# Kernel tuning notes

Measured on AMD Instinct MI355X. Metric: run time of the kernel, lower is better.

## Reference

```python
import jax, jax.numpy as jnp
import numpy as np

EPS = 1e-6      # torch F.pairwise_distance default eps (added to the difference)
MARGIN = 0.5


def setup_inputs() -> dict:
    key = jax.random.key(0)
    k1, k2 = jax.random.split(key)
    batch = jax.random.normal(k1, (8192, 1024), dtype=jnp.float32)
    positive = jax.random.normal(k2, (1024,), dtype=jnp.float32)
    return {"batch": batch, "positive": positive}


def _loss(batch, positive):
    n, d = batch.shape
    # torch pairwise_distance(x, y) = ||x - y + eps||_2, so
    # ||a - b + eps||^2 = ||a||^2 + ||b||^2 - 2 a.b + 2*eps*(sum(a) - sum(b)) + d*eps^2
    sq = jnp.sum(batch * batch, axis=-1)                 # [n]
    dots = batch @ batch.T                               # [n, n] GEMM
    sums = jnp.sum(batch, axis=-1)                       # [n]
    d2 = (sq[:, None] + sq[None, :] - 2.0 * dots
          + 2.0 * EPS * (sums[:, None] - sums[None, :]) + d * EPS * EPS)
    # exclude self (the python loop concatenates batch[:i], batch[i+1:])
    neg_inf = jnp.asarray(-jnp.inf, d2.dtype)
    d2_masked = jnp.where(jnp.eye(n, dtype=bool), neg_inf, d2)
    max_neg = jnp.sqrt(jnp.maximum(jnp.max(d2_masked, axis=-1), 0.0))  # [n]
    # distance anchor -> positive (with torch eps convention)
    diff = batch - positive[None, :] + EPS
    pos_dist = jnp.sqrt(jnp.sum(diff * diff, axis=-1))   # [n]
    losses = jax.nn.relu(pos_dist - max_neg + MARGIN)    # [n]
    # anchors exactly equal to the positive are skipped in the original loop
    valid = ~jnp.all(batch == positive[None, :], axis=-1)
    cnt = jnp.sum(valid.astype(losses.dtype))
    return jnp.sum(jnp.where(valid, losses, 0.0)) / cnt


def reference(batch, positive):
    return _loss(batch, positive)
```

## Files before the change

kernel.cpp:

```cpp
#include <hip/hip_runtime.h>
#include <hip/hip_bf16.h>


#define NROWS 8192
#define DIM   1024
#define BT    256
#define BK    64
#define NKT   (DIM / BK)
#define NBT   (NROWS / BT)
#define NTRI  (NBT * (NBT + 1) / 2)

constexpr float EPS = 1e-6f;
constexpr float MARGIN = 0.5f;

typedef __attribute__((ext_vector_type(8))) short short8;
typedef __attribute__((ext_vector_type(4))) float f32x4;

__device__ __forceinline__ unsigned short f2bf_rne(float f) {
    unsigned u = __float_as_uint(f);
    u += 0x7fffu + ((u >> 16) & 1u);
    return (unsigned short)(u >> 16);
}

__global__ void prep_kernel(const float* __restrict__ X, const float* __restrict__ P,
                            unsigned short* __restrict__ Xb,
                            float* __restrict__ cj, float* __restrict__ basei,
                            float* __restrict__ posd, int* __restrict__ valid)
{
    const int tid  = threadIdx.x;
    const int w    = tid >> 6;
    const int lane = tid & 63;
    const int row  = blockIdx.x * 4 + w;
    const float* xr = X + (size_t)row * DIM;

    float sq = 0.f, sm = 0.f, pd = 0.f;
    bool eq = true;
    #pragma unroll
    for (int it = 0; it < 4; ++it) {
        const int idx = it * 256 + lane * 4;
        const float4 x = *(const float4*)(xr + idx);
        const float4 p = *(const float4*)(P + idx);
        sq += x.x*x.x + x.y*x.y + x.z*x.z + x.w*x.w;
        sm += x.x + x.y + x.z + x.w;
        const float d0 = x.x - p.x + EPS, d1 = x.y - p.y + EPS;
        const float d2 = x.z - p.z + EPS, d3 = x.w - p.w + EPS;
        pd += d0*d0 + d1*d1 + d2*d2 + d3*d3;
        eq = eq && (x.x == p.x) && (x.y == p.y) && (x.z == p.z) && (x.w == p.w);
        ushort4 b;
        b.x = f2bf_rne(x.x); b.y = f2bf_rne(x.y); b.z = f2bf_rne(x.z); b.w = f2bf_rne(x.w);
        *(ushort4*)(Xb + (size_t)row * DIM + idx) = b;
    }
    #pragma unroll
    for (int off = 32; off >= 1; off >>= 1) {
        sq += __shfl_xor(sq, off);
        sm += __shfl_xor(sm, off);
        pd += __shfl_xor(pd, off);
    }
    const bool alleq = __all(eq);
    if (lane == 0) {
        cj[row]    = sq - 2.f * EPS * sm;
        basei[row] = sq + 2.f * EPS * sm + (float)DIM * EPS * EPS;
        posd[row]  = sqrtf(pd);
        valid[row] = alleq ? 0 : 1;
    }
}

__global__ __launch_bounds__(512, 2) void gemm_max_kernel(
        const unsigned short* __restrict__ Xb,
        const float* __restrict__ cj,
        float* __restrict__ partmax)
{
    __shared__ alignas(16) unsigned short lds[2][4][8192];
    __shared__ float partrow[4][BT];
    __shared__ float partcol[2][BT];

    const int tid  = threadIdx.x;
    const int lane = tid & 63;
    const int wid  = tid >> 6;
    const int wm   = wid >> 2;
    const int wn   = wid & 3;
    const int l15  = lane & 15;
    const int lk   = lane >> 4;
    const int cx0  = lk ^ (l15 & 7);
    const int cx1  = (4 + lk) ^ (l15 & 7);

    const int t0 = (blockIdx.x & 7) * (NTRI / 8) + (blockIdx.x >> 3);
    int bm = (int)(32.5f - sqrtf(1056.25f - 2.f * (float)t0));
    if (bm < 0) bm = 0;
    if (bm > NBT - 1) bm = NBT - 1;
    while (bm > 0 && (65 * bm - bm * bm) / 2 > t0) --bm;
    while ((65 * (bm + 1) - (bm + 1) * (bm + 1)) / 2 <= t0) ++bm;
    const int bn = bm + (t0 - (65 * bm - bm * bm) / 2);
    const bool diag = (bm == bn);
    const int Mbase = bm * BT, Nbase = bn * BT;

    f32x4 acc[8][4];
    #pragma unroll
    for (int m = 0; m < 8; ++m)
        #pragma unroll
        for (int n = 0; n < 4; ++n)
            acc[m][n] = (f32x4){0.f, 0.f, 0.f, 0.f};

    #define STAGE(BUF, SLOT, GBASE, KT) do {                                                  \
        _Pragma("unroll")                                                                     \
        for (int inst_ = 0; inst_ < 2; ++inst_) {                                             \
            const int q_ = inst_ * 512 + tid;                                                 \
            const int r_ = q_ >> 3;                                                           \
            const int c_ = (q_ & 7) ^ (r_ & 7);                                               \
            const unsigned short* src_ = Xb + (size_t)((GBASE) + r_) * DIM + (KT) * BK + c_ * 8; \
            unsigned short* dst_ = &lds[BUF][SLOT][(inst_ * 512 + wid * 64) * 8];             \
            __builtin_amdgcn_global_load_lds((const __attribute__((address_space(1))) void*)src_, \
                                             (__attribute__((address_space(3))) void*)dst_, 16, 0, 0); \
        }                                                                                     \
    } while (0)

    STAGE(0, 0, Mbase, 0); STAGE(0, 1, Mbase + 128, 0);
    STAGE(0, 2, Nbase, 0); STAGE(0, 3, Nbase + 128, 0);
    STAGE(1, 0, Mbase, 1); STAGE(1, 1, Mbase + 128, 1);
    STAGE(1, 2, Nbase, 1); STAGE(1, 3, Nbase + 128, 1);
    asm volatile("s_waitcnt vmcnt(8)" ::: "memory");
    __builtin_amdgcn_s_barrier();
    __builtin_amdgcn_sched_barrier(0);

    const int cl0 = (wn & 1) * 64;

    short8 bf0[4], bf1[4], af[8];
    {
        const unsigned short* B0 = &lds[0][2 + (wn >> 1)][0];
        #pragma unroll
        for (int nt = 0; nt < 2; ++nt) {
            bf0[nt * 2]     = *(const short8*)(B0 + ((cl0 + nt * 16 + l15) * 8 + cx0) * 8);
            bf0[nt * 2 + 1] = *(const short8*)(B0 + ((cl0 + nt * 16 + l15) * 8 + cx1) * 8);
        }
    }

    for (int kt = 0; kt < NKT; ++kt) {
        const int b = kt & 1;
        const unsigned short* Ah = &lds[b][wm][0];
        const unsigned short* Bh = &lds[b][2 + (wn >> 1)][0];
        const unsigned short* Bn = &lds[b ^ 1][2 + (wn >> 1)][0];
        const bool st = (kt + 2 < NKT);
        const int kp = kt + 2;

        #pragma unroll
        for (int mt = 0; mt < 4; ++mt) {
            af[mt * 2]     = *(const short8*)(Ah + ((mt * 16 + l15) * 8 + cx0) * 8);
            af[mt * 2 + 1] = *(const short8*)(Ah + ((mt * 16 + l15) * 8 + cx1) * 8);
        }
        __builtin_amdgcn_s_setprio(1);
        #pragma unroll
        for (int ks = 0; ks < 2; ++ks)
            #pragma unroll
            for (int mt = 0; mt < 4; ++mt)
                #pragma unroll
                for (int nt = 0; nt < 2; ++nt)
                    acc[mt][nt] = __builtin_amdgcn_mfma_f32_16x16x32_bf16(af[mt*2+ks], bf0[nt*2+ks], acc[mt][nt], 0, 0, 0);
        __builtin_amdgcn_s_setprio(0);
        __builtin_amdgcn_s_barrier();

        #pragma unroll
        for (int nt = 0; nt < 2; ++nt) {
            bf1[nt * 2]     = *(const short8*)(Bh + ((cl0 + 32 + nt * 16 + l15) * 8 + cx0) * 8);
            bf1[nt * 2 + 1] = *(const short8*)(Bh + ((cl0 + 32 + nt * 16 + l15) * 8 + cx1) * 8);
        }
        __builtin_amdgcn_s_setprio(1);
        #pragma unroll
        for (int ks = 0; ks < 2; ++ks)
            #pragma unroll
            for (int mt = 0; mt < 4; ++mt)
                #pragma unroll
                for (int nt = 0; nt < 2; ++nt)
                    acc[mt][2+nt] = __builtin_amdgcn_mfma_f32_16x16x32_bf16(af[mt*2+ks], bf1[nt*2+ks], acc[mt][2+nt], 0, 0, 0);
        __builtin_amdgcn_s_setprio(0);
        __builtin_amdgcn_s_barrier();

        #pragma unroll
        for (int mt = 0; mt < 4; ++mt) {
            af[mt * 2]     = *(const short8*)(Ah + ((64 + mt * 16 + l15) * 8 + cx0) * 8);
            af[mt * 2 + 1] = *(const short8*)(Ah + ((64 + mt * 16 + l15) * 8 + cx1) * 8);
        }
        if (st) { STAGE(b, 2, Nbase, kp); STAGE(b, 3, Nbase + 128, kp); }
        __builtin_amdgcn_s_setprio(1);
        #pragma unroll
        for (int ks = 0; ks < 2; ++ks)
            #pragma unroll
            for (int mt = 0; mt < 4; ++mt)
                #pragma unroll
                for (int nt = 0; nt < 2; ++nt)
                    acc[4+mt][2+nt] = __builtin_amdgcn_mfma_f32_16x16x32_bf16(af[mt*2+ks], bf1[nt*2+ks], acc[4+mt][2+nt], 0, 0, 0);
        __builtin_amdgcn_s_setprio(0);
        __builtin_amdgcn_s_barrier();

        if (st) { STAGE(b, 0, Mbase, kp); STAGE(b, 1, Mbase + 128, kp); }
        __builtin_amdgcn_s_setprio(1);
        #pragma unroll
        for (int ks = 0; ks < 2; ++ks)
            #pragma unroll
            for (int mt = 0; mt < 4; ++mt)
                #pragma unroll
                for (int nt = 0; nt < 2; ++nt)
                    acc[4+mt][nt] = __builtin_amdgcn_mfma_f32_16x16x32_bf16(af[mt*2+ks], bf0[nt*2+ks], acc[4+mt][nt], 0, 0, 0);
        __builtin_amdgcn_s_setprio(0);

        if (kt <= NKT - 3)      asm volatile("s_waitcnt vmcnt(8)" ::: "memory");
        else                    asm volatile("s_waitcnt vmcnt(0)" ::: "memory");
        if (kt < NKT - 1) {
            #pragma unroll
            for (int nt = 0; nt < 2; ++nt) {
                bf0[nt * 2]     = *(const short8*)(Bn + ((cl0 + nt * 16 + l15) * 8 + cx0) * 8);
                bf0[nt * 2 + 1] = *(const short8*)(Bn + ((cl0 + nt * 16 + l15) * 8 + cx1) * 8);
            }
        }
        __builtin_amdgcn_s_barrier();
        __builtin_amdgcn_sched_barrier(0);
    }
    #undef STAGE

    float cv[4];
    #pragma unroll
    for (int n = 0; n < 4; ++n)
        cv[n] = cj[Nbase + wn * 64 + n * 16 + l15];

    #pragma unroll
    for (int m = 0; m < 8; ++m) {
        #pragma unroll
        for (int r = 0; r < 4; ++r) {
            const int lrow = wm * 128 + m * 16 + lk * 4 + r;
            float v = -__builtin_inff();
            #pragma unroll
            for (int n = 0; n < 4; ++n) {
                float val = cv[n] - 2.f * acc[m][n][r];
                if (diag && lrow == wn * 64 + n * 16 + l15) val = -__builtin_inff();
                v = fmaxf(v, val);
            }
            #pragma unroll
            for (int off = 8; off >= 1; off >>= 1)
                v = fmaxf(v, __shfl_xor(v, off));
            if (l15 == 0) partrow[wn][lrow] = v;
        }
    }

    if (!diag) {
        float vt[4];
        #pragma unroll
        for (int n = 0; n < 4; ++n) vt[n] = -__builtin_inff();
        #pragma unroll
        for (int m = 0; m < 8; ++m) {
            #pragma unroll
            for (int r = 0; r < 4; ++r) {
                const float ci = cj[Mbase + wm * 128 + m * 16 + lk * 4 + r];
                #pragma unroll
                for (int n = 0; n < 4; ++n)
                    vt[n] = fmaxf(vt[n], ci - 2.f * acc[m][n][r]);
            }
        }
        #pragma unroll
        for (int n = 0; n < 4; ++n) {
            vt[n] = fmaxf(vt[n], __shfl_xor(vt[n], 16));
            vt[n] = fmaxf(vt[n], __shfl_xor(vt[n], 32));
            if (lk == 0) partcol[wm][wn * 64 + n * 16 + l15] = vt[n];
        }
    }
    __syncthreads();

    if (tid < BT) {
        const float v = fmaxf(fmaxf(partrow[0][tid], partrow[1][tid]),
                              fmaxf(partrow[2][tid], partrow[3][tid]));
        partmax[(size_t)bn * NROWS + Mbase + tid] = v;
    } else if (!diag) {
        const int c = tid - BT;
        partmax[(size_t)bm * NROWS + Nbase + c] = fmaxf(partcol[0][c], partcol[1][c]);
    }
}

__global__ void finalize1_kernel(const float* __restrict__ partmax,
                                 const float* __restrict__ basei,
                                 const float* __restrict__ posd,
                                 const int* __restrict__ valid,
                                 float* __restrict__ partials)
{
    const int tid = threadIdx.x;
    const int row = blockIdx.x * 256 + tid;
    float m = -__builtin_inff();
    #pragma unroll 8
    for (int p = 0; p < NBT; ++p)
        m = fmaxf(m, partmax[(size_t)p * NROWS + row]);
    const float d2 = m + basei[row];
    const float mn = sqrtf(fmaxf(d2, 0.f));
    float loss = fmaxf(posd[row] - mn + MARGIN, 0.f);
    float cnt = 1.f;
    if (!valid[row]) { loss = 0.f; cnt = 0.f; }
    #pragma unroll
    for (int off = 32; off >= 1; off >>= 1) {
        loss += __shfl_xor(loss, off);
        cnt  += __shfl_xor(cnt, off);
    }
    __shared__ float sl[4], sc[4];
    const int w = tid >> 6, lane = tid & 63;
    if (lane == 0) { sl[w] = loss; sc[w] = cnt; }
    __syncthreads();
    if (tid == 0) {
        partials[blockIdx.x * 2]     = sl[0] + sl[1] + sl[2] + sl[3];
        partials[blockIdx.x * 2 + 1] = sc[0] + sc[1] + sc[2] + sc[3];
    }
}

__global__ void finalize2_kernel(const float* __restrict__ partials, float* __restrict__ out)
{
    const int tid = threadIdx.x;
    float l = 0.f, c = 0.f;
    if (tid < 32) { l = partials[tid * 2]; c = partials[tid * 2 + 1]; }
    #pragma unroll
    for (int off = 32; off >= 1; off >>= 1) {
        l += __shfl_xor(l, off);
        c += __shfl_xor(c, off);
    }
    if (tid == 0) out[0] = l / c;
}

extern "C" void kernel_launch(void* const* d_in, const int* in_sizes, int n_in,
                              void* d_out, int out_size, void* d_ws, size_t ws_size,
                              hipStream_t stream)
{
    const float* X = (const float*)d_in[0];
    const float* P = (const float*)d_in[1];
    float* out = (float*)d_out;
    char* ws = (char*)d_ws;

    unsigned short* Xb = (unsigned short*)ws;
    size_t off = (size_t)NROWS * DIM * sizeof(unsigned short);
    float* cj    = (float*)(ws + off);  off += (size_t)NROWS * 4;
    float* basei = (float*)(ws + off);  off += (size_t)NROWS * 4;
    float* posd  = (float*)(ws + off);  off += (size_t)NROWS * 4;
    int*   valid = (int*)(ws + off);    off += (size_t)NROWS * 4;
    float* partmax = (float*)(ws + off); off += (size_t)NBT * NROWS * 4;
    float* partials = (float*)(ws + off);

    prep_kernel<<<NROWS / 4, 256, 0, stream>>>(X, P, Xb, cj, basei, posd, valid);
    gemm_max_kernel<<<NTRI, 512, 0, stream>>>(Xb, cj, partmax);
    finalize1_kernel<<<NROWS / 256, 256, 0, stream>>>(partmax, basei, posd, valid, partials);
    finalize2_kernel<<<1, 64, 0, stream>>>(partials, out);
}
```

Before: 122.3 us.

## Reassign warp A-rows across slots and spread staging across GEMM phases

Each warp's A fragments are remapped so that the first half comes from LDS slot 0 and the second half from slot 1, rather than 128 contiguous rows from a single slot. Global-to-LDS staging of the next k-tile is split into smaller pieces placed between the four MFMA phases. Next-tile B fragments are prefetched into a separate register set after a partial vmcnt wait, and barriers with explicit lgkmcnt waits are added before each phase. The aim is finer-grained overlap of loads with MFMA work. In exchange there are more barriers, extra registers, and the epilogue row mapping has to follow the new layout.

```diff
diff --git a/kernel.cpp b/kernel.cpp
--- a/kernel.cpp
+++ b/kernel.cpp
@@ -83,6 +83,8 @@
     const int lk   = lane >> 4;
     const int cx0  = lk ^ (l15 & 7);
     const int cx1  = (4 + lk) ^ (l15 & 7);
+    const int bslot = 2 + (wn >> 1);
+    const int cl0   = (wn & 1) * 64;
 
     const int t0 = (blockIdx.x & 7) * (NTRI / 8) + (blockIdx.x >> 3);
     int bm = (int)(32.5f - sqrtf(1056.25f - 2.f * (float)t0));
@@ -120,13 +122,10 @@
     STAGE(1, 2, Nbase, 1); STAGE(1, 3, Nbase + 128, 1);
     asm volatile("s_waitcnt vmcnt(8)" ::: "memory");
     __builtin_amdgcn_s_barrier();
-    __builtin_amdgcn_sched_barrier(0);
-
-    const int cl0 = (wn & 1) * 64;
-
-    short8 bf0[4], bf1[4], af[8];
+
+    short8 af[8], bf0[4], bf1[4], bf0n[4];
     {
-        const unsigned short* B0 = &lds[0][2 + (wn >> 1)][0];
+        const unsigned short* B0 = &lds[0][bslot][0];
         #pragma unroll
         for (int nt = 0; nt < 2; ++nt) {
             bf0[nt * 2]     = *(const short8*)(B0 + ((cl0 + nt * 16 + l15) * 8 + cx0) * 8);
@@ -136,17 +135,21 @@
 
     for (int kt = 0; kt < NKT; ++kt) {
         const int b = kt & 1;
-        const unsigned short* Ah = &lds[b][wm][0];
-        const unsigned short* Bh = &lds[b][2 + (wn >> 1)][0];
-        const unsigned short* Bn = &lds[b ^ 1][2 + (wn >> 1)][0];
         const bool st = (kt + 2 < NKT);
         const int kp = kt + 2;
+        const unsigned short* A0 = &lds[b][0][0];
+        const unsigned short* A1 = &lds[b][1][0];
+        const unsigned short* Bh = &lds[b][bslot][0];
+        const unsigned short* Bn = &lds[b ^ 1][bslot][0];
 
         #pragma unroll
         for (int mt = 0; mt < 4; ++mt) {
-            af[mt * 2]     = *(const short8*)(Ah + ((mt * 16 + l15) * 8 + cx0) * 8);
-            af[mt * 2 + 1] = *(const short8*)(Ah + ((mt * 16 + l15) * 8 + cx1) * 8);
-        }
+            const int row = wm * 64 + mt * 16 + l15;
+            af[mt * 2]     = *(const short8*)(A0 + (row * 8 + cx0) * 8);
+            af[mt * 2 + 1] = *(const short8*)(A0 + (row * 8 + cx1) * 8);
+        }
+        __builtin_amdgcn_s_barrier();
+        asm volatile("s_waitcnt lgkmcnt(0)" ::: "memory");
         __builtin_amdgcn_s_setprio(1);
         #pragma unroll
         for (int ks = 0; ks < 2; ++ks)
@@ -163,6 +166,9 @@
             bf1[nt * 2]     = *(const short8*)(Bh + ((cl0 + 32 + nt * 16 + l15) * 8 + cx0) * 8);
             bf1[nt * 2 + 1] = *(const short8*)(Bh + ((cl0 + 32 + nt * 16 + l15) * 8 + cx1) * 8);
         }
+        if (st) STAGE(b, 0, Mbase, kp);
+        __builtin_amdgcn_s_barrier();
+        asm volatile("s_waitcnt lgkmcnt(0)" ::: "memory");
         __builtin_amdgcn_s_setprio(1);
         #pragma unroll
         for (int ks = 0; ks < 2; ++ks)
@@ -176,10 +182,13 @@
 
         #pragma unroll
         for (int mt = 0; mt < 4; ++mt) {
-            af[mt * 2]     = *(const short8*)(Ah + ((64 + mt * 16 + l15) * 8 + cx0) * 8);
-            af[mt * 2 + 1] = *(const short8*)(Ah + ((64 + mt * 16 + l15) * 8 + cx1) * 8);
-        }
-        if (st) { STAGE(b, 2, Nbase, kp); STAGE(b, 3, Nbase + 128, kp); }
+            const int row = wm * 64 + mt * 16 + l15;
+            af[mt * 2]     = *(const short8*)(A1 + (row * 8 + cx0) * 8);
+            af[mt * 2 + 1] = *(const short8*)(A1 + (row * 8 + cx1) * 8);
+        }
+        if (st) STAGE(b, 2, Nbase, kp);
+        __builtin_amdgcn_s_barrier();
+        asm volatile("s_waitcnt lgkmcnt(0)" ::: "memory");
         __builtin_amdgcn_s_setprio(1);
         #pragma unroll
         for (int ks = 0; ks < 2; ++ks)
@@ -191,7 +200,17 @@
         __builtin_amdgcn_s_setprio(0);
         __builtin_amdgcn_s_barrier();
 
-        if (st) { STAGE(b, 0, Mbase, kp); STAGE(b, 1, Mbase + 128, kp); }
+        if (st) { STAGE(b, 1, Mbase + 128, kp); STAGE(b, 3, Nbase + 128, kp); }
+        if (kt < NKT - 1) {
+            asm volatile("s_waitcnt vmcnt(4)" ::: "memory");
+            #pragma unroll
+            for (int nt = 0; nt < 2; ++nt) {
+                bf0n[nt * 2]     = *(const short8*)(Bn + ((cl0 + nt * 16 + l15) * 8 + cx0) * 8);
+                bf0n[nt * 2 + 1] = *(const short8*)(Bn + ((cl0 + nt * 16 + l15) * 8 + cx1) * 8);
+            }
+        }
+        __builtin_amdgcn_s_barrier();
+        asm volatile("s_waitcnt lgkmcnt(0)" ::: "memory");
         __builtin_amdgcn_s_setprio(1);
         #pragma unroll
         for (int ks = 0; ks < 2; ++ks)
@@ -201,18 +220,10 @@
                 for (int nt = 0; nt < 2; ++nt)
                     acc[4+mt][nt] = __builtin_amdgcn_mfma_f32_16x16x32_bf16(af[mt*2+ks], bf0[nt*2+ks], acc[4+mt][nt], 0, 0, 0);
         __builtin_amdgcn_s_setprio(0);
-
-        if (kt <= NKT - 3)      asm volatile("s_waitcnt vmcnt(8)" ::: "memory");
-        else                    asm volatile("s_waitcnt vmcnt(0)" ::: "memory");
-        if (kt < NKT - 1) {
-            #pragma unroll
-            for (int nt = 0; nt < 2; ++nt) {
-                bf0[nt * 2]     = *(const short8*)(Bn + ((cl0 + nt * 16 + l15) * 8 + cx0) * 8);
-                bf0[nt * 2 + 1] = *(const short8*)(Bn + ((cl0 + nt * 16 + l15) * 8 + cx1) * 8);
-            }
-        }
-        __builtin_amdgcn_s_barrier();
-        __builtin_amdgcn_sched_barrier(0);
+        __builtin_amdgcn_s_barrier();
+
+        #pragma unroll
+        for (int i = 0; i < 4; ++i) bf0[i] = bf0n[i];
     }
     #undef STAGE
 
@@ -223,9 +234,10 @@
 
     #pragma unroll
     for (int m = 0; m < 8; ++m) {
+        const int rbase = (m < 4) ? (wm * 64 + m * 16) : (128 + wm * 64 + (m - 4) * 16);
         #pragma unroll
         for (int r = 0; r < 4; ++r) {
-            const int lrow = wm * 128 + m * 16 + lk * 4 + r;
+            const int lrow = rbase + lk * 4 + r;
             float v = -__builtin_inff();
             #pragma unroll
             for (int n = 0; n < 4; ++n) {
@@ -246,9 +258,10 @@
         for (int n = 0; n < 4; ++n) vt[n] = -__builtin_inff();
         #pragma unroll
         for (int m = 0; m < 8; ++m) {
+            const int rbase = (m < 4) ? (wm * 64 + m * 16) : (128 + wm * 64 + (m - 4) * 16);
             #pragma unroll
             for (int r = 0; r < 4; ++r) {
-                const float ci = cj[Mbase + wm * 128 + m * 16 + lk * 4 + r];
+                const float ci = cj[Mbase + rbase + lk * 4 + r];
                 #pragma unroll
                 for (int n = 0; n < 4; ++n)
                     vt[n] = fmaxf(vt[n], ci - 2.f * acc[m][n][r]);
```

Result: slower. 128.3 us (+4.9%).
